# Kernel optimization log

Measured on AMD Instinct MI355X. Metric: run time of the kernel, lower is better.

The kernel has to match this reference:

```python
import jax, jax.numpy as jnp
import numpy as np

NUM_USERS = 100000
NUM_ITEMS = 50000
DIM = 64
HOP = 3
NNZ = 4_000_000
BATCH = 4096
NUM_NEG = 8
N = NUM_USERS + NUM_ITEMS


def setup_inputs() -> dict:
    key = jax.random.key(0)
    ks = jax.random.split(key, 8)
    user_emb = jax.random.normal(ks[0], (NUM_USERS, DIM), dtype=jnp.float32) * 0.1
    item_emb = jax.random.normal(ks[1], (NUM_ITEMS, DIM), dtype=jnp.float32) * 0.1
    # normalized-Laplacian-like small positive values
    A_vals = jax.random.uniform(ks[2], (NNZ,), dtype=jnp.float32) * 0.02
    A_rows = jax.random.randint(ks[3], (NNZ,), 0, N, dtype=jnp.int32)
    A_cols = jax.random.randint(ks[4], (NNZ,), 0, N, dtype=jnp.int32)
    users = jax.random.randint(ks[5], (BATCH,), 0, NUM_USERS, dtype=jnp.int32)
    items = jax.random.randint(ks[6], (BATCH,), 0, NUM_ITEMS, dtype=jnp.int32)
    negatives = jax.random.randint(ks[7], (NUM_NEG * BATCH,), 0, NUM_ITEMS, dtype=jnp.int32)
    return {"user_emb": user_emb, "item_emb": item_emb, "A_vals": A_vals,
            "A_rows": A_rows, "A_cols": A_cols,
            "users": users, "items": items, "negatives": negatives}


def _computer(user_emb, item_emb, A_vals, A_rows, A_cols):
    # LightGCN propagation: x_{k+1} = A @ x_k, mean over hops 0..HOP
    all_emb = jnp.concatenate([user_emb, item_emb], axis=0)  # [N, D]
    x = all_emb
    acc = all_emb
    for _ in range(HOP):
        # SpMM: gather source rows, scale by edge value, scatter-add to dest
        msgs = A_vals[:, None] * x[A_cols]                      # [nnz, D]
        x = jax.ops.segment_sum(msgs, A_rows, num_segments=N)   # [N, D]
        acc = acc + x
    light_out = acc / jnp.asarray(HOP + 1, dtype=all_emb.dtype)
    return light_out[:NUM_USERS], light_out[NUM_USERS:]


def reference(user_emb, item_emb, A_vals, A_rows, A_cols, users, items, negatives):
    all_users_emb, all_items_emb = _computer(user_emb, item_emb, A_vals, A_rows, A_cols)
    users_emb = all_users_emb[users]          # [B, D]
    items_emb = all_items_emb[items]          # [B, D]
    neg_item_embs = all_items_emb[negatives]  # [NUM_NEG*B, D]
    pos_scores = jnp.sum(users_emb * items_emb, axis=1)  # [B]
    pos_exp = jnp.exp(pos_scores)
    neg_k = jnp.sum(users_emb[None, :, :] * neg_item_embs.reshape(NUM_NEG, BATCH, DIM), axis=-1)  # [NUM_NEG, B]
    neg_exp = jnp.sum(jnp.exp(neg_k), axis=0)  # [B]
    info_nce = jnp.mean(-jnp.log(pos_exp / (pos_exp + neg_exp)))
    return info_nce
```

## Files before the change

kernel.cpp:

```cpp
#include <hip/hip_runtime.h>
#include <hip/hip_bf16.h>
#include <hip/hip_fp8.h>


#define NUM_USERS 100000
#define NUM_ITEMS 50000
#define NTOT      150000
#define DIM       64
#define NNZ_C     4000000
#define BATCH     4096
#define NUM_NEG   8
#define NSLICE    (BATCH + BATCH + NUM_NEG * BATCH)

#define RPB        192
#define NBUCKET    ((NTOT + RPB - 1) / RPB)
#define CAP        5632
#define CAPC       6080
#define BIN_BLOCKS 1024
#define EDGES_PER_BIN ((NNZ_C + BIN_BLOCKS - 1) / BIN_BLOCKS)

using fp8t = __hip_fp8_e4m3;

typedef unsigned int u32x4 __attribute__((ext_vector_type(4)));
typedef float        f32x2 __attribute__((ext_vector_type(2)));

__device__ __forceinline__ float f8dec(unsigned char b) {
    fp8t h; h.__x = (__hip_fp8_storage_t)b; return (float)h;
}
__device__ __forceinline__ unsigned char f8enc(float f) {
    fp8t h(f); return (unsigned char)h.__x;
}

__device__ __forceinline__ void fp8x4_fma(unsigned int q, float w, float* a) {
#if __has_builtin(__builtin_amdgcn_cvt_pk_f32_fp8)
    f32x2 lo = __builtin_amdgcn_cvt_pk_f32_fp8((int)q, false);
    f32x2 hi = __builtin_amdgcn_cvt_pk_f32_fp8((int)q, true);
    a[0] = fmaf(w, lo.x, a[0]);
    a[1] = fmaf(w, lo.y, a[1]);
    a[2] = fmaf(w, hi.x, a[2]);
    a[3] = fmaf(w, hi.y, a[3]);
#else
    a[0] = fmaf(w, f8dec((unsigned char)(q       & 0xFF)), a[0]);
    a[1] = fmaf(w, f8dec((unsigned char)((q>>8)  & 0xFF)), a[1]);
    a[2] = fmaf(w, f8dec((unsigned char)((q>>16) & 0xFF)), a[2]);
    a[3] = fmaf(w, f8dec((unsigned char)((q>>24) & 0xFF)), a[3]);
#endif
}

__global__ void convert_concat(const float* __restrict__ ue, const float* __restrict__ ie,
                               unsigned char* __restrict__ x0, float* __restrict__ loss_accum) {
    int i = blockIdx.x * blockDim.x + threadIdx.x;
    if (i == 0) loss_accum[0] = 0.0f;
    if (i >= NTOT * DIM / 4) return;
    float4 v = (i * 4 < NUM_USERS * DIM)
                   ? ((const float4*)ue)[i]
                   : ((const float4*)ie)[i - NUM_USERS * DIM / 4];
    uchar4 o;
    o.x = f8enc(v.x); o.y = f8enc(v.y); o.z = f8enc(v.z); o.w = f8enc(v.w);
    ((uchar4*)x0)[i] = o;
}

__global__ void init_bcur(int* __restrict__ bcur) {
    int i = blockIdx.x * blockDim.x + threadIdx.x;
    if (i < NBUCKET) bcur[i] = i * CAP;
}

__global__ void __launch_bounds__(256) bin_k(const int* __restrict__ rows,
                                             const int* __restrict__ cols,
                                             const float* __restrict__ vals,
                                             int* __restrict__ bcur,
                                             int2* __restrict__ brec) {
    __shared__ int2 stage[EDGES_PER_BIN];
    __shared__ int  pdst[EDGES_PER_BIN];
    __shared__ int  lh[NBUCKET], lofs[NBUCKET], gbase[NBUCKET];
    __shared__ int  sm[256];
    int t = threadIdx.x;
    for (int i = t; i < NBUCKET; i += 256) lh[i] = 0;
    __syncthreads();
    int e0 = blockIdx.x * EDGES_PER_BIN;
    int e1 = e0 + EDGES_PER_BIN; if (e1 > NNZ_C) e1 = NNZ_C;
    #pragma unroll 4
    for (int e = e0 + t; e < e1; e += 256)
        atomicAdd(&lh[__builtin_nontemporal_load(rows + e) / RPB], 1);
    __syncthreads();
    {
        const int K = (NBUCKET + 255) / 256;
        int loc[4];
        int s = 0;
        for (int k = 0; k < K; ++k) {
            int i = t * K + k;
            loc[k] = (i < NBUCKET) ? lh[i] : 0;
            s += loc[k];
        }
        sm[t] = s;
        __syncthreads();
        for (int o = 1; o < 256; o <<= 1) {
            int v = (t >= o) ? sm[t - o] : 0;
            __syncthreads();
            sm[t] += v;
            __syncthreads();
        }
        int run = sm[t] - s;
        for (int k = 0; k < K; ++k) {
            int i = t * K + k;
            if (i < NBUCKET) lofs[i] = run;
            run += loc[k];
        }
    }
    __syncthreads();
    for (int i = t; i < NBUCKET; i += 256) {
        int c = lh[i];
        gbase[i] = c ? atomicAdd(&bcur[i], c) : 0;
        lh[i] = 0;
    }
    __syncthreads();
    #pragma unroll 2
    for (int e = e0 + t; e < e1; e += 256) {
        int r = __builtin_nontemporal_load(rows + e);
        int c = __builtin_nontemporal_load(cols + e);
        float v = __builtin_nontemporal_load(vals + e);
        int b = r / RPB;
        int rank = atomicAdd(&lh[b], 1);
        int j = lofs[b] + rank;
        stage[j] = make_int2(((r - b * RPB) << 18) | c, __float_as_int(v));
        pdst[j]  = gbase[b] + rank;
    }
    __syncthreads();
    int cnt = e1 - e0;
    for (int j = t; j < cnt; j += 256)
        brec[pdst[j]] = stage[j];
}

__global__ void csr_fix_k(const int2* __restrict__ brec, const int* __restrict__ bcur,
                          unsigned int* __restrict__ crec, int2* __restrict__ rp2) {
    __shared__ int lh[RPB], lb[RPB], lc[RPB], sm[RPB];
    int b = blockIdx.x;
    int t = threadIdx.x;
    int s = b * CAP, e = bcur[b];
    int cnt = e - s;
    int cb = b * CAPC;
    if (t < RPB) lh[t] = 0;
    __syncthreads();
    for (int j = t; j < cnt; j += 256)
        atomicAdd(&lh[(brec[s + j].x >> 18) & 255], 1);
    __syncthreads();
    int cnt4 = 0;
    if (t < RPB) { cnt4 = (lh[t] + 3) & ~3; sm[t] = cnt4; }
    __syncthreads();
    for (int o = 1; o < RPB; o <<= 1) {
        int v = 0;
        if (t < RPB && t >= o) v = sm[t - o];
        __syncthreads();
        if (t < RPB) sm[t] += v;
        __syncthreads();
    }
    if (t < RPB) {
        int ex4 = sm[t] - cnt4;
        lb[t] = ex4;
        lc[t] = 0;
        int row = b * RPB + t;
        if (row < NTOT) rp2[row] = make_int2(cb + ex4, cb + ex4 + lh[t]);
    }
    __syncthreads();
    for (int j = t; j < cnt; j += 256) {
        int2 rc = brec[s + j];
        int rl = (rc.x >> 18) & 255;
        int pos = atomicAdd(&lc[rl], 1);
        float v = __int_as_float(rc.y);
        unsigned int v14 = (unsigned int)lrintf(v * 524288.0f);
        if (v14 > 16383u) v14 = 16383u;
        crec[cb + lb[rl] + pos] = (v14 << 18) | (unsigned int)(rc.x & 0x3FFFF);
    }
    if (t < RPB) {
        int base = cb + lb[t];
        int c4 = (lh[t] + 3) & ~3;
        for (int q = lh[t]; q < c4; ++q) crec[base + q] = 0u;
    }
}

__device__ __forceinline__ void spmm_row_v3(const unsigned char* __restrict__ x,
                                            const unsigned int* __restrict__ crec,
                                            int s, int e, int lane, float* acc) {
    const float c19 = 1.9073486328125e-6f;
    int g  = lane >> 4;
    int dq = (lane & 15) * 4;
    acc[0] = acc[1] = acc[2] = acc[3] = 0.0f;
    int e4 = s + ((e - s + 3) & ~3);
    for (int j = s + 4 * g; j < e4; j += 16) {
        u32x4 p = __builtin_nontemporal_load((const u32x4*)(crec + j));
        unsigned int q0 = *(const unsigned int*)(x + (p.x & 0x3FFFFu) * DIM + dq);
        unsigned int q1 = *(const unsigned int*)(x + (p.y & 0x3FFFFu) * DIM + dq);
        unsigned int q2 = *(const unsigned int*)(x + (p.z & 0x3FFFFu) * DIM + dq);
        unsigned int q3 = *(const unsigned int*)(x + (p.w & 0x3FFFFu) * DIM + dq);
        float w0 = (float)(p.x >> 18) * c19;
        float w1 = (float)(p.y >> 18) * c19;
        float w2 = (float)(p.z >> 18) * c19;
        float w3 = (float)(p.w >> 18) * c19;
        fp8x4_fma(q0, w0, acc);
        fp8x4_fma(q1, w1, acc);
        fp8x4_fma(q2, w2, acc);
        fp8x4_fma(q3, w3, acc);
    }
    acc[0] += __shfl_xor(acc[0], 16, 64);
    acc[1] += __shfl_xor(acc[1], 16, 64);
    acc[2] += __shfl_xor(acc[2], 16, 64);
    acc[3] += __shfl_xor(acc[3], 16, 64);
    acc[0] += __shfl_xor(acc[0], 32, 64);
    acc[1] += __shfl_xor(acc[1], 32, 64);
    acc[2] += __shfl_xor(acc[2], 32, 64);
    acc[3] += __shfl_xor(acc[3], 32, 64);
}

__device__ __forceinline__ void spmm_store(unsigned char* __restrict__ y, int row,
                                           int lane, const float* acc) {
    if (lane < 16) {
        uchar4 o;
        o.x = f8enc(acc[0] * 16.0f);
        o.y = f8enc(acc[1] * 16.0f);
        o.z = f8enc(acc[2] * 16.0f);
        o.w = f8enc(acc[3] * 16.0f);
        *(uchar4*)(y + row * DIM + lane * 4) = o;
    }
}

__global__ void spmm_k(const unsigned char* __restrict__ x, const int2* __restrict__ rp2,
                       const unsigned int* __restrict__ crec, unsigned char* __restrict__ y) {
    int row  = (blockIdx.x * blockDim.x + threadIdx.x) >> 6;
    int lane = threadIdx.x & 63;
    if (row >= NTOT) return;
    int2 se = rp2[row];
    float acc[4];
    spmm_row_v3(x, crec, se.x, se.y, lane, acc);
    spmm_store(y, row, lane, acc);
}

__global__ void spmm_sliced_k(const unsigned char* __restrict__ x, const int2* __restrict__ rp2,
                              const unsigned int* __restrict__ crec,
                              const int* __restrict__ users, const int* __restrict__ items,
                              const int* __restrict__ negs, unsigned char* __restrict__ y) {
    int w    = (blockIdx.x * blockDim.x + threadIdx.x) >> 6;
    int lane = threadIdx.x & 63;
    if (w >= NSLICE) return;
    int row = (w < BATCH)     ? users[w]
            : (w < 2 * BATCH) ? NUM_USERS + items[w - BATCH]
                              : NUM_USERS + negs[w - 2 * BATCH];
    int2 se = rp2[row];
    float acc[4];
    spmm_row_v3(x, crec, se.x, se.y, lane, acc);
    spmm_store(y, row, lane, acc);
}

__global__ void loss_k(const unsigned char* __restrict__ x0, const unsigned char* __restrict__ x1,
                       const unsigned char* __restrict__ x2, const unsigned char* __restrict__ x3,
                       const int* __restrict__ users, const int* __restrict__ items,
                       const int* __restrict__ negs, float* __restrict__ loss_accum) {
    int w    = (blockIdx.x * blockDim.x + threadIdx.x) >> 6;
    int lane = threadIdx.x & 63;
    if (w >= BATCH) return;
    auto rowv = [&](int r) -> float {
        int o = r * DIM + lane;
        return 0.25f * f8dec(x0[o]) + 0.015625f * f8dec(x1[o]) +
               9.765625e-4f * f8dec(x2[o]) + 6.103515625e-5f * f8dec(x3[o]);
    };
    float ue = rowv(users[w]);
    float ie = rowv(NUM_USERS + items[w]);
    float p = ue * ie;
    for (int o = 32; o > 0; o >>= 1) p += __shfl_xor(p, o, 64);
    float pe = expf(p);
    float ne = 0.0f;
    for (int k = 0; k < NUM_NEG; ++k) {
        float q = ue * rowv(NUM_USERS + negs[k * BATCH + w]);
        for (int o = 32; o > 0; o >>= 1) q += __shfl_xor(q, o, 64);
        ne += expf(q);
    }
    if (lane == 0) atomicAdd(loss_accum, logf((pe + ne) / pe));
}

__global__ void finalize_k(const float* __restrict__ loss_accum, float* __restrict__ out) {
    out[0] = loss_accum[0] * (1.0f / BATCH);
}

__global__ void sentinel_k(float* __restrict__ out) {
    out[0] = -1.0f;
}

extern "C" void kernel_launch(void* const* d_in, const int* in_sizes, int n_in,
                              void* d_out, int out_size, void* d_ws, size_t ws_size,
                              hipStream_t stream) {
    const float* user_emb = (const float*)d_in[0];
    const float* item_emb = (const float*)d_in[1];
    const float* A_vals   = (const float*)d_in[2];
    const int*   A_rows   = (const int*)d_in[3];
    const int*   A_cols   = (const int*)d_in[4];
    const int*   users    = (const int*)d_in[5];
    const int*   items    = (const int*)d_in[6];
    const int*   negs     = (const int*)d_in[7];
    float* out = (float*)d_out;

    char* ws = (char*)d_ws;
    size_t off = 0;
    auto carve = [&](size_t bytes) -> char* {
        char* p = ws + off;
        off = (off + bytes + 255) & ~(size_t)255;
        return p;
    };
    unsigned char* x0 = (unsigned char*)carve((size_t)NTOT * DIM);
    unsigned char* x1 = (unsigned char*)carve((size_t)NTOT * DIM);
    unsigned char* x2 = (unsigned char*)carve((size_t)NTOT * DIM);
    unsigned char* x3 = (unsigned char*)carve((size_t)NTOT * DIM);
    int2*  brec       = (int2*)carve((size_t)NBUCKET * CAP * 8);
    unsigned int* crec= (unsigned int*)carve((size_t)NBUCKET * CAPC * 4 + 1024);
    int2*  rp2        = (int2*)carve((size_t)NTOT * 8);
    int*   bcur       = (int*)carve((size_t)NBUCKET * 4);
    float* loss_accum = (float*)carve(256);

    if (off > ws_size) {
        sentinel_k<<<1, 1, 0, stream>>>(out);
        return;
    }

    convert_concat<<<(NTOT * DIM / 4 + 255) / 256, 256, 0, stream>>>(user_emb, item_emb, x0, loss_accum);

    init_bcur<<<(NBUCKET + 255) / 256, 256, 0, stream>>>(bcur);
    bin_k<<<BIN_BLOCKS, 256, 0, stream>>>(A_rows, A_cols, A_vals, bcur, brec);
    csr_fix_k<<<NBUCKET, 256, 0, stream>>>(brec, bcur, crec, rp2);

    const int spmm_blocks = (NTOT * 64 + 255) / 256;
    spmm_k<<<spmm_blocks, 256, 0, stream>>>(x0, rp2, crec, x1);
    spmm_k<<<spmm_blocks, 256, 0, stream>>>(x1, rp2, crec, x2);
    spmm_sliced_k<<<(NSLICE * 64 + 255) / 256, 256, 0, stream>>>(x2, rp2, crec, users, items, negs, x3);

    loss_k<<<(BATCH * 64 + 255) / 256, 256, 0, stream>>>(x0, x1, x2, x3, users, items, negs, loss_accum);
    finalize_k<<<1, 1, 0, stream>>>(loss_accum, out);
}
```

Before: 440.2 us.

## Restructure edge binning with compact split records and padded bucket counters

The binning kernel now scatters edges straight to global memory instead of staging them in shared memory. It uses vectorized int4 loads, twice as many blocks, and no local prefix scan. Each bucket record is split into a 4-byte packed value/column word, quantized at binning time, and a 1-byte local row id, replacing the 8-byte int2. This cuts the traffic csr_fix_k reads and lets it use vectorized loads. Bucket counters are padded to 64 bytes to avoid atomic contention on shared cache lines, and their init is folded into the conversion kernel to drop a launch. The trade-off is that global writes from binning become scattered rather than grouped by bucket, which may hurt write coalescing.

```diff
diff --git a/kernel.cpp b/kernel.cpp
--- a/kernel.cpp
+++ b/kernel.cpp
@@ -16,12 +16,14 @@
 #define NBUCKET    ((NTOT + RPB - 1) / RPB)
 #define CAP        5632
 #define CAPC       6080
-#define BIN_BLOCKS 1024
-#define EDGES_PER_BIN ((NNZ_C + BIN_BLOCKS - 1) / BIN_BLOCKS)
+#define BIN_BLOCKS 2048
+#define EPB        1956
 
 using fp8t = __hip_fp8_e4m3;
 
 typedef unsigned int u32x4 __attribute__((ext_vector_type(4)));
+typedef int          i32x4 __attribute__((ext_vector_type(4)));
+typedef float        f32x4 __attribute__((ext_vector_type(4)));
 typedef float        f32x2 __attribute__((ext_vector_type(2)));
 
 __device__ __forceinline__ float f8dec(unsigned char b) {
@@ -48,9 +50,11 @@
 }
 
 __global__ void convert_concat(const float* __restrict__ ue, const float* __restrict__ ie,
-                               unsigned char* __restrict__ x0, float* __restrict__ loss_accum) {
+                               unsigned char* __restrict__ x0, float* __restrict__ loss_accum,
+                               int* __restrict__ bcur) {
     int i = blockIdx.x * blockDim.x + threadIdx.x;
     if (i == 0) loss_accum[0] = 0.0f;
+    if (i < NBUCKET) bcur[i * 16] = i * CAP;
     if (i >= NTOT * DIM / 4) return;
     float4 v = (i * 4 < NUM_USERS * DIM)
                    ? ((const float4*)ue)[i]
@@ -60,89 +64,92 @@
     ((uchar4*)x0)[i] = o;
 }
 
-__global__ void init_bcur(int* __restrict__ bcur) {
-    int i = blockIdx.x * blockDim.x + threadIdx.x;
-    if (i < NBUCKET) bcur[i] = i * CAP;
-}
-
 __global__ void __launch_bounds__(256) bin_k(const int* __restrict__ rows,
                                              const int* __restrict__ cols,
                                              const float* __restrict__ vals,
                                              int* __restrict__ bcur,
-                                             int2* __restrict__ brec) {
-    __shared__ int2 stage[EDGES_PER_BIN];
-    __shared__ int  pdst[EDGES_PER_BIN];
-    __shared__ int  lh[NBUCKET], lofs[NBUCKET], gbase[NBUCKET];
-    __shared__ int  sm[256];
+                                             unsigned int* __restrict__ brec4,
+                                             unsigned char* __restrict__ brow) {
+    __shared__ int lh[NBUCKET], gbase[NBUCKET];
     int t = threadIdx.x;
     for (int i = t; i < NBUCKET; i += 256) lh[i] = 0;
     __syncthreads();
-    int e0 = blockIdx.x * EDGES_PER_BIN;
-    int e1 = e0 + EDGES_PER_BIN; if (e1 > NNZ_C) e1 = NNZ_C;
-    #pragma unroll 4
-    for (int e = e0 + t; e < e1; e += 256)
-        atomicAdd(&lh[__builtin_nontemporal_load(rows + e) / RPB], 1);
-    __syncthreads();
-    {
-        const int K = (NBUCKET + 255) / 256;
-        int loc[4];
-        int s = 0;
-        for (int k = 0; k < K; ++k) {
-            int i = t * K + k;
-            loc[k] = (i < NBUCKET) ? lh[i] : 0;
-            s += loc[k];
-        }
-        sm[t] = s;
-        __syncthreads();
-        for (int o = 1; o < 256; o <<= 1) {
-            int v = (t >= o) ? sm[t - o] : 0;
-            __syncthreads();
-            sm[t] += v;
-            __syncthreads();
-        }
-        int run = sm[t] - s;
-        for (int k = 0; k < K; ++k) {
-            int i = t * K + k;
-            if (i < NBUCKET) lofs[i] = run;
-            run += loc[k];
-        }
+    int e0 = blockIdx.x * EPB;
+    int e1 = e0 + EPB; if (e1 > NNZ_C) e1 = NNZ_C;
+    for (int e = e0 + t * 4; e < e1; e += 1024) {
+        i32x4 r = __builtin_nontemporal_load((const i32x4*)(rows + e));
+        atomicAdd(&lh[r.x / RPB], 1);
+        atomicAdd(&lh[r.y / RPB], 1);
+        atomicAdd(&lh[r.z / RPB], 1);
+        atomicAdd(&lh[r.w / RPB], 1);
     }
     __syncthreads();
     for (int i = t; i < NBUCKET; i += 256) {
         int c = lh[i];
-        gbase[i] = c ? atomicAdd(&bcur[i], c) : 0;
+        gbase[i] = c ? atomicAdd(&bcur[i * 16], c) : 0;
         lh[i] = 0;
     }
     __syncthreads();
-    #pragma unroll 2
-    for (int e = e0 + t; e < e1; e += 256) {
-        int r = __builtin_nontemporal_load(rows + e);
-        int c = __builtin_nontemporal_load(cols + e);
-        float v = __builtin_nontemporal_load(vals + e);
-        int b = r / RPB;
-        int rank = atomicAdd(&lh[b], 1);
-        int j = lofs[b] + rank;
-        stage[j] = make_int2(((r - b * RPB) << 18) | c, __float_as_int(v));
-        pdst[j]  = gbase[b] + rank;
-    }
-    __syncthreads();
-    int cnt = e1 - e0;
-    for (int j = t; j < cnt; j += 256)
-        brec[pdst[j]] = stage[j];
-}
-
-__global__ void csr_fix_k(const int2* __restrict__ brec, const int* __restrict__ bcur,
+    for (int e = e0 + t * 4; e < e1; e += 1024) {
+        i32x4 r = __builtin_nontemporal_load((const i32x4*)(rows + e));
+        i32x4 c = __builtin_nontemporal_load((const i32x4*)(cols + e));
+        f32x4 v = __builtin_nontemporal_load((const f32x4*)(vals + e));
+        {
+            int b = r.x / RPB;
+            int dst = gbase[b] + atomicAdd(&lh[b], 1);
+            unsigned int v14 = (unsigned int)lrintf(v.x * 524288.0f);
+            if (v14 > 16383u) v14 = 16383u;
+            brec4[dst] = (v14 << 18) | (unsigned int)c.x;
+            brow[dst]  = (unsigned char)(r.x - b * RPB);
+        }
+        {
+            int b = r.y / RPB;
+            int dst = gbase[b] + atomicAdd(&lh[b], 1);
+            unsigned int v14 = (unsigned int)lrintf(v.y * 524288.0f);
+            if (v14 > 16383u) v14 = 16383u;
+            brec4[dst] = (v14 << 18) | (unsigned int)c.y;
+            brow[dst]  = (unsigned char)(r.y - b * RPB);
+        }
+        {
+            int b = r.z / RPB;
+            int dst = gbase[b] + atomicAdd(&lh[b], 1);
+            unsigned int v14 = (unsigned int)lrintf(v.z * 524288.0f);
+            if (v14 > 16383u) v14 = 16383u;
+            brec4[dst] = (v14 << 18) | (unsigned int)c.z;
+            brow[dst]  = (unsigned char)(r.z - b * RPB);
+        }
+        {
+            int b = r.w / RPB;
+            int dst = gbase[b] + atomicAdd(&lh[b], 1);
+            unsigned int v14 = (unsigned int)lrintf(v.w * 524288.0f);
+            if (v14 > 16383u) v14 = 16383u;
+            brec4[dst] = (v14 << 18) | (unsigned int)c.w;
+            brow[dst]  = (unsigned char)(r.w - b * RPB);
+        }
+    }
+}
+
+__global__ void csr_fix_k(const unsigned int* __restrict__ brec4,
+                          const unsigned char* __restrict__ brow,
+                          const int* __restrict__ bcur,
                           unsigned int* __restrict__ crec, int2* __restrict__ rp2) {
     __shared__ int lh[RPB], lb[RPB], lc[RPB], sm[RPB];
     int b = blockIdx.x;
     int t = threadIdx.x;
-    int s = b * CAP, e = bcur[b];
+    int s = b * CAP, e = bcur[b * 16];
     int cnt = e - s;
     int cb = b * CAPC;
     if (t < RPB) lh[t] = 0;
     __syncthreads();
-    for (int j = t; j < cnt; j += 256)
-        atomicAdd(&lh[(brec[s + j].x >> 18) & 255], 1);
+    int n4 = cnt >> 2;
+    const uchar4* bp = (const uchar4*)(brow + s);
+    for (int j = t; j < n4; j += 256) {
+        uchar4 r = bp[j];
+        atomicAdd(&lh[r.x], 1); atomicAdd(&lh[r.y], 1);
+        atomicAdd(&lh[r.z], 1); atomicAdd(&lh[r.w], 1);
+    }
+    for (int j = (n4 << 2) + t; j < cnt; j += 256)
+        atomicAdd(&lh[brow[s + j]], 1);
     __syncthreads();
     int cnt4 = 0;
     if (t < RPB) { cnt4 = (lh[t] + 3) & ~3; sm[t] = cnt4; }
@@ -162,15 +169,21 @@
         if (row < NTOT) rp2[row] = make_int2(cb + ex4, cb + ex4 + lh[t]);
     }
     __syncthreads();
-    for (int j = t; j < cnt; j += 256) {
-        int2 rc = brec[s + j];
-        int rl = (rc.x >> 18) & 255;
+    const uint4* qp = (const uint4*)(brec4 + s);
+    for (int j = t; j < n4; j += 256) {
+        uchar4 r = bp[j];
+        uint4  q = qp[j];
+        int p0 = atomicAdd(&lc[r.x], 1); crec[cb + lb[r.x] + p0] = q.x;
+        int p1 = atomicAdd(&lc[r.y], 1); crec[cb + lb[r.y] + p1] = q.y;
+        int p2 = atomicAdd(&lc[r.z], 1); crec[cb + lb[r.z] + p2] = q.z;
+        int p3 = atomicAdd(&lc[r.w], 1); crec[cb + lb[r.w] + p3] = q.w;
+    }
+    for (int j = (n4 << 2) + t; j < cnt; j += 256) {
+        int rl = brow[s + j];
         int pos = atomicAdd(&lc[rl], 1);
-        float v = __int_as_float(rc.y);
-        unsigned int v14 = (unsigned int)lrintf(v * 524288.0f);
-        if (v14 > 16383u) v14 = 16383u;
-        crec[cb + lb[rl] + pos] = (v14 << 18) | (unsigned int)(rc.x & 0x3FFFF);
-    }
+        crec[cb + lb[rl] + pos] = brec4[s + j];
+    }
+    __syncthreads();
     if (t < RPB) {
         int base = cb + lb[t];
         int c4 = (lh[t] + 3) & ~3;
@@ -308,10 +321,11 @@
     unsigned char* x1 = (unsigned char*)carve((size_t)NTOT * DIM);
     unsigned char* x2 = (unsigned char*)carve((size_t)NTOT * DIM);
     unsigned char* x3 = (unsigned char*)carve((size_t)NTOT * DIM);
-    int2*  brec       = (int2*)carve((size_t)NBUCKET * CAP * 8);
-    unsigned int* crec= (unsigned int*)carve((size_t)NBUCKET * CAPC * 4 + 1024);
+    unsigned int* brec4 = (unsigned int*)carve((size_t)NBUCKET * CAP * 4);
+    unsigned char* brow = (unsigned char*)carve((size_t)NBUCKET * CAP);
+    unsigned int* crec  = (unsigned int*)carve((size_t)NBUCKET * CAPC * 4 + 1024);
     int2*  rp2        = (int2*)carve((size_t)NTOT * 8);
-    int*   bcur       = (int*)carve((size_t)NBUCKET * 4);
+    int*   bcur       = (int*)carve((size_t)NBUCKET * 64);
     float* loss_accum = (float*)carve(256);
 
     if (off > ws_size) {
@@ -319,11 +333,10 @@
         return;
     }
 
-    convert_concat<<<(NTOT * DIM / 4 + 255) / 256, 256, 0, stream>>>(user_emb, item_emb, x0, loss_accum);
-
-    init_bcur<<<(NBUCKET + 255) / 256, 256, 0, stream>>>(bcur);
-    bin_k<<<BIN_BLOCKS, 256, 0, stream>>>(A_rows, A_cols, A_vals, bcur, brec);
-    csr_fix_k<<<NBUCKET, 256, 0, stream>>>(brec, bcur, crec, rp2);
+    convert_concat<<<(NTOT * DIM / 4 + 255) / 256, 256, 0, stream>>>(user_emb, item_emb, x0, loss_accum, bcur);
+
+    bin_k<<<BIN_BLOCKS, 256, 0, stream>>>(A_rows, A_cols, A_vals, bcur, brec4, brow);
+    csr_fix_k<<<NBUCKET, 256, 0, stream>>>(brec4, brow, bcur, crec, rp2);
 
     const int spmm_blocks = (NTOT * 64 + 255) / 256;
     spmm_k<<<spmm_blocks, 256, 0, stream>>>(x0, rp2, crec, x1);
```

After: 520.3 us. 18.2% more time.

## Restructure edge binning: cache rows in registers, drop pdst array, pad bucket counters

Applied to the files above, without the earlier changes.

The binning kernel now loads each edge's row index once into registers and reuses it for both the histogram and the scatter pass, instead of reading rows from global memory twice. It drops the shared pdst array by recomputing destinations from the bucket offset, which shrinks shared memory and may raise occupancy. Value quantization moves from csr_fix into the bin kernel, and records now carry the global row. Bucket cursors are spaced 64 bytes apart to reduce atomic contention, and their initialization is folded into convert_concat so one launch is removed. The extra registers per thread and the changed record encoding add risk.

```diff
diff --git a/kernel.cpp b/kernel.cpp
--- a/kernel.cpp
+++ b/kernel.cpp
@@ -17,7 +17,8 @@
 #define CAP        5632
 #define CAPC       6080
 #define BIN_BLOCKS 1024
-#define EDGES_PER_BIN ((NNZ_C + BIN_BLOCKS - 1) / BIN_BLOCKS)
+#define EPB        ((NNZ_C + BIN_BLOCKS - 1) / BIN_BLOCKS)
+#define KEDGE      ((EPB + 255) / 256)
 
 using fp8t = __hip_fp8_e4m3;
 
@@ -48,9 +49,11 @@
 }
 
 __global__ void convert_concat(const float* __restrict__ ue, const float* __restrict__ ie,
-                               unsigned char* __restrict__ x0, float* __restrict__ loss_accum) {
+                               unsigned char* __restrict__ x0, float* __restrict__ loss_accum,
+                               int* __restrict__ bcur) {
     int i = blockIdx.x * blockDim.x + threadIdx.x;
     if (i == 0) loss_accum[0] = 0.0f;
+    if (i < NBUCKET) bcur[i * 16] = i * CAP;
     if (i >= NTOT * DIM / 4) return;
     float4 v = (i * 4 < NUM_USERS * DIM)
                    ? ((const float4*)ue)[i]
@@ -60,39 +63,40 @@
     ((uchar4*)x0)[i] = o;
 }
 
-__global__ void init_bcur(int* __restrict__ bcur) {
-    int i = blockIdx.x * blockDim.x + threadIdx.x;
-    if (i < NBUCKET) bcur[i] = i * CAP;
-}
-
 __global__ void __launch_bounds__(256) bin_k(const int* __restrict__ rows,
                                              const int* __restrict__ cols,
                                              const float* __restrict__ vals,
                                              int* __restrict__ bcur,
                                              int2* __restrict__ brec) {
-    __shared__ int2 stage[EDGES_PER_BIN];
-    __shared__ int  pdst[EDGES_PER_BIN];
-    __shared__ int  lh[NBUCKET], lofs[NBUCKET], gbase[NBUCKET];
-    __shared__ int  sm[256];
+    __shared__ int2 stage[EPB];
+    __shared__ int  lh[NBUCKET], gbase[NBUCKET];
+    __shared__ unsigned short lofs[NBUCKET];
     int t = threadIdx.x;
+    int* sm = (int*)stage;
+    int e0 = blockIdx.x * EPB;
+    int e1 = e0 + EPB; if (e1 > NNZ_C) e1 = NNZ_C;
     for (int i = t; i < NBUCKET; i += 256) lh[i] = 0;
-    __syncthreads();
-    int e0 = blockIdx.x * EDGES_PER_BIN;
-    int e1 = e0 + EDGES_PER_BIN; if (e1 > NNZ_C) e1 = NNZ_C;
-    #pragma unroll 4
-    for (int e = e0 + t; e < e1; e += 256)
-        atomicAdd(&lh[__builtin_nontemporal_load(rows + e) / RPB], 1);
+    int er[KEDGE];
+    #pragma unroll
+    for (int k = 0; k < KEDGE; ++k) {
+        int e = e0 + k * 256 + t;
+        er[k] = (e < e1) ? __builtin_nontemporal_load(rows + e) : -1;
+    }
+    __syncthreads();
+    #pragma unroll
+    for (int k = 0; k < KEDGE; ++k)
+        if (er[k] >= 0) atomicAdd(&lh[er[k] / RPB], 1);
     __syncthreads();
     {
         const int K = (NBUCKET + 255) / 256;
         int loc[4];
-        int s = 0;
+        int ssum = 0;
         for (int k = 0; k < K; ++k) {
             int i = t * K + k;
             loc[k] = (i < NBUCKET) ? lh[i] : 0;
-            s += loc[k];
+            ssum += loc[k];
         }
-        sm[t] = s;
+        sm[t] = ssum;
         __syncthreads();
         for (int o = 1; o < 256; o <<= 1) {
             int v = (t >= o) ? sm[t - o] : 0;
@@ -100,35 +104,42 @@
             sm[t] += v;
             __syncthreads();
         }
-        int run = sm[t] - s;
+        int run = sm[t] - ssum;
         for (int k = 0; k < K; ++k) {
             int i = t * K + k;
-            if (i < NBUCKET) lofs[i] = run;
+            if (i < NBUCKET) lofs[i] = (unsigned short)run;
             run += loc[k];
         }
     }
     __syncthreads();
     for (int i = t; i < NBUCKET; i += 256) {
         int c = lh[i];
-        gbase[i] = c ? atomicAdd(&bcur[i], c) : 0;
+        gbase[i] = c ? atomicAdd(&bcur[i * 16], c) : 0;
         lh[i] = 0;
     }
     __syncthreads();
-    #pragma unroll 2
-    for (int e = e0 + t; e < e1; e += 256) {
-        int r = __builtin_nontemporal_load(rows + e);
-        int c = __builtin_nontemporal_load(cols + e);
-        float v = __builtin_nontemporal_load(vals + e);
-        int b = r / RPB;
-        int rank = atomicAdd(&lh[b], 1);
-        int j = lofs[b] + rank;
-        stage[j] = make_int2(((r - b * RPB) << 18) | c, __float_as_int(v));
-        pdst[j]  = gbase[b] + rank;
+    #pragma unroll
+    for (int k = 0; k < KEDGE; ++k) {
+        int e = e0 + k * 256 + t;
+        if (er[k] >= 0) {
+            int   c = __builtin_nontemporal_load(cols + e);
+            float v = __builtin_nontemporal_load(vals + e);
+            int b = er[k] / RPB;
+            int rank = atomicAdd(&lh[b], 1);
+            int j = (int)lofs[b] + rank;
+            unsigned int v14 = (unsigned int)lrintf(v * 524288.0f);
+            if (v14 > 16383u) v14 = 16383u;
+            stage[j] = make_int2((int)((v14 << 18) | (unsigned int)c), er[k]);
+        }
     }
     __syncthreads();
     int cnt = e1 - e0;
-    for (int j = t; j < cnt; j += 256)
-        brec[pdst[j]] = stage[j];
+    for (int j = t; j < cnt; j += 256) {
+        int2 rc = stage[j];
+        int b = rc.y / RPB;
+        int dst = gbase[b] + (j - (int)lofs[b]);
+        brec[dst] = rc;
+    }
 }
 
 __global__ void csr_fix_k(const int2* __restrict__ brec, const int* __restrict__ bcur,
@@ -136,13 +147,14 @@
     __shared__ int lh[RPB], lb[RPB], lc[RPB], sm[RPB];
     int b = blockIdx.x;
     int t = threadIdx.x;
-    int s = b * CAP, e = bcur[b];
+    int s = b * CAP, e = bcur[b * 16];
     int cnt = e - s;
     int cb = b * CAPC;
+    int rbase = b * RPB;
     if (t < RPB) lh[t] = 0;
     __syncthreads();
     for (int j = t; j < cnt; j += 256)
-        atomicAdd(&lh[(brec[s + j].x >> 18) & 255], 1);
+        atomicAdd(&lh[brec[s + j].y - rbase], 1);
     __syncthreads();
     int cnt4 = 0;
     if (t < RPB) { cnt4 = (lh[t] + 3) & ~3; sm[t] = cnt4; }
@@ -158,19 +170,17 @@
         int ex4 = sm[t] - cnt4;
         lb[t] = ex4;
         lc[t] = 0;
-        int row = b * RPB + t;
+        int row = rbase + t;
         if (row < NTOT) rp2[row] = make_int2(cb + ex4, cb + ex4 + lh[t]);
     }
     __syncthreads();
     for (int j = t; j < cnt; j += 256) {
         int2 rc = brec[s + j];
-        int rl = (rc.x >> 18) & 255;
+        int rl = rc.y - rbase;
         int pos = atomicAdd(&lc[rl], 1);
-        float v = __int_as_float(rc.y);
-        unsigned int v14 = (unsigned int)lrintf(v * 524288.0f);
-        if (v14 > 16383u) v14 = 16383u;
-        crec[cb + lb[rl] + pos] = (v14 << 18) | (unsigned int)(rc.x & 0x3FFFF);
-    }
+        crec[cb + lb[rl] + pos] = (unsigned int)rc.x;
+    }
+    __syncthreads();
     if (t < RPB) {
         int base = cb + lb[t];
         int c4 = (lh[t] + 3) & ~3;
@@ -311,7 +321,7 @@
     int2*  brec       = (int2*)carve((size_t)NBUCKET * CAP * 8);
     unsigned int* crec= (unsigned int*)carve((size_t)NBUCKET * CAPC * 4 + 1024);
     int2*  rp2        = (int2*)carve((size_t)NTOT * 8);
-    int*   bcur       = (int*)carve((size_t)NBUCKET * 4);
+    int*   bcur       = (int*)carve((size_t)NBUCKET * 64);
     float* loss_accum = (float*)carve(256);
 
     if (off > ws_size) {
@@ -319,9 +329,8 @@
         return;
     }
 
-    convert_concat<<<(NTOT * DIM / 4 + 255) / 256, 256, 0, stream>>>(user_emb, item_emb, x0, loss_accum);
-
-    init_bcur<<<(NBUCKET + 255) / 256, 256, 0, stream>>>(bcur);
+    convert_concat<<<(NTOT * DIM / 4 + 255) / 256, 256, 0, stream>>>(user_emb, item_emb, x0, loss_accum, bcur);
+
     bin_k<<<BIN_BLOCKS, 256, 0, stream>>>(A_rows, A_cols, A_vals, bcur, brec);
     csr_fix_k<<<NBUCKET, 256, 0, stream>>>(brec, bcur, crec, rp2);
 
```

Result: slower. 458.7 us (+4.2%).
